# Kernel tuning notes

Measured on AMD Instinct MI355X. Metric: run time of the kernel, lower is better.

## Reference

```python
import jax, jax.numpy as jnp
import numpy as np

E = 800000
D = 64
N = 50000

def setup_inputs() -> dict:
    key = jax.random.key(0)
    k1, k2 = jax.random.split(key)
    src = jax.random.normal(k1, (E, D), dtype=jnp.float32)
    index = jax.random.randint(k2, (E,), 0, N, dtype=jnp.int64)
    return {"src": src, "index": index, "dim": 0, "dim_size": N}

def reference(src, index, dim, dim_size):
    # scatter-mean along dim=0: segment sum divided by per-segment counts
    # (torch_scatter mean clamps count to >= 1 so empty segments stay 0).
    sums = jax.ops.segment_sum(src, index, num_segments=dim_size)  # [N, D]
    counts = jax.ops.segment_sum(jnp.ones((src.shape[0],), dtype=src.dtype),
                                 index, num_segments=dim_size)      # [N]
    denom = jnp.maximum(counts, 1.0)
    return sums / denom[:, None]
```

## Files before the change

kernel.cpp:

```cpp
#include <hip/hip_runtime.h>


typedef unsigned int u32;

__global__ void zero_u32_kernel(u32* __restrict__ p, int n) {
    int i = blockIdx.x * blockDim.x + threadIdx.x;
    int stride = gridDim.x * blockDim.x;
    for (; i < n; i += stride) p[i] = 0u;
}

__global__ void hist_kernel(const int* __restrict__ idx, u32* __restrict__ hist, int E) {
    int i = blockIdx.x * blockDim.x + threadIdx.x;
    int stride = gridDim.x * blockDim.x;
    for (; i < E; i += stride) atomicAdd(&hist[idx[i]], 1u);
}


__global__ void scanA_kernel(const u32* __restrict__ hist, u32* __restrict__ pb, int N) {
    const int b = blockIdx.x, t = threadIdx.x;
    const int base = b * 1024 + t * 4;
    u32 s = 0;
#pragma unroll
    for (int k = 0; k < 4; ++k) { int i = base + k; if (i < N) s += hist[i]; }
#pragma unroll
    for (int d = 32; d > 0; d >>= 1) s += __shfl_down(s, d);
    __shared__ u32 wsum[4];
    int lane = t & 63, wid = t >> 6;
    if (lane == 0) wsum[wid] = s;
    __syncthreads();
    if (t == 0) pb[b] = wsum[0] + wsum[1] + wsum[2] + wsum[3];
}

__global__ void scanB_kernel(u32* __restrict__ pb, u32* __restrict__ ofs, int nblk, int N) {
    if (threadIdx.x == 0 && blockIdx.x == 0) {
        u32 run = 0;
        for (int b = 0; b < nblk; ++b) { u32 v = pb[b]; pb[b] = run; run += v; }
        ofs[N] = run;
    }
}

__global__ void scanC_kernel(const u32* __restrict__ hist, const u32* __restrict__ pb,
                             u32* __restrict__ ofs, int N) {
    const int b = blockIdx.x, t = threadIdx.x;
    const int base = b * 1024 + t * 4;
    u32 v[4]; u32 s = 0;
#pragma unroll
    for (int k = 0; k < 4; ++k) { int i = base + k; v[k] = (i < N) ? hist[i] : 0u; s += v[k]; }
    u32 inc = s;
    int lane = t & 63, wid = t >> 6;
#pragma unroll
    for (int d = 1; d < 64; d <<= 1) { u32 x = __shfl_up(inc, d); if (lane >= d) inc += x; }
    __shared__ u32 wsum[4];
    if (lane == 63) wsum[wid] = inc;
    __syncthreads();
    u32 waveBase = 0;
    for (int w = 0; w < wid; ++w) waveBase += wsum[w];
    u32 run = pb[b] + waveBase + (inc - s);
#pragma unroll
    for (int k = 0; k < 4; ++k) { int i = base + k; if (i < N) ofs[i] = run; run += v[k]; }
}

__global__ void scatter_perm_kernel(const int* __restrict__ idx, const u32* __restrict__ ofs,
                                    u32* __restrict__ ctr, u32* __restrict__ perm, int E) {
    int i = blockIdx.x * blockDim.x + threadIdx.x;
    int stride = gridDim.x * blockDim.x;
    for (; i < E; i += stride) {
        int n = idx[i];
        u32 pos = ofs[n] + atomicAdd(&ctr[n], 1u);
        perm[pos] = (u32)i;
    }
}

__global__ void gather_mean_kernel(const float* __restrict__ src, const u32* __restrict__ perm,
                                   const u32* __restrict__ ofs, float* __restrict__ out, int N) {
    int seg = blockIdx.x * (blockDim.x >> 6) + (threadIdx.x >> 6);
    int lane = threadIdx.x & 63;
    if (seg >= N) return;
    u32 beg = ofs[seg], end = ofs[seg + 1];
    int cnt = (int)(end - beg);
    float acc = 0.f;
    u32 j = beg;
    for (; j + 2 <= end; j += 2) {
        u32 e0 = perm[j], e1 = perm[j + 1];
        acc += src[(long)e0 * 64 + lane];
        acc += src[(long)e1 * 64 + lane];
    }
    if (j < end) acc += src[(long)perm[j] * 64 + lane];
    float inv = 1.0f / (float)(cnt > 1 ? cnt : 1);
    out[(long)seg * 64 + lane] = acc * inv;
}

__global__ void zero_f4_kernel(float4* __restrict__ p, long n4) {
    long i = (long)blockIdx.x * blockDim.x + threadIdx.x;
    long stride = (long)gridDim.x * blockDim.x;
    float4 z = make_float4(0.f, 0.f, 0.f, 0.f);
    for (; i < n4; i += stride) p[i] = z;
}
__global__ void scatter_add_kernel(const float4* __restrict__ src4, const int* __restrict__ idx,
                                   float* __restrict__ out, float* __restrict__ cnt, int E) {
    long t = (long)blockIdx.x * blockDim.x + threadIdx.x;
    long total = (long)E * 16;
    long stride = (long)gridDim.x * blockDim.x;
    for (; t < total; t += stride) {
        int e = (int)(t >> 4), c4 = (int)(t & 15);
        int n = idx[e];
        float4 v = src4[(long)e * 16 + c4];
        float* o = out + (long)n * 64 + c4 * 4;
        atomicAdd(o + 0, v.x); atomicAdd(o + 1, v.y);
        atomicAdd(o + 2, v.z); atomicAdd(o + 3, v.w);
        if (c4 == 0) atomicAdd(cnt + n, 1.0f);
    }
}
__global__ void divide_kernel(float4* __restrict__ out4, const float* __restrict__ cnt, int N) {
    long t = (long)blockIdx.x * blockDim.x + threadIdx.x;
    long total = (long)N * 16;
    long stride = (long)gridDim.x * blockDim.x;
    for (; t < total; t += stride) {
        int n = (int)(t >> 4);
        float inv = 1.0f / fmaxf(cnt[n], 1.0f);
        float4 v = out4[t];
        v.x *= inv; v.y *= inv; v.z *= inv; v.w *= inv;
        out4[t] = v;
    }
}

extern "C" void kernel_launch(void* const* d_in, const int* in_sizes, int n_in,
                              void* d_out, int out_size, void* d_ws, size_t ws_size,
                              hipStream_t stream) {
    const float* src = (const float*)d_in[0];
    const int*   idx = (const int*)d_in[1];
    float* out = (float*)d_out;

    const int E = in_sizes[1];
    const int D = in_sizes[0] / E;
    const int N = out_size / D;
    const int BLK = 256;

    const size_t OFS_OFF  = 0;
    const size_t HIST_OFF = (size_t)(N + 64) & ~63ul;
    const size_t PB_OFF   = HIST_OFF + (((size_t)N + 64) & ~63ul);
    const size_t PERM_OFF = PB_OFF + 64;
    const size_t NEED = (PERM_OFF + (size_t)E) * 4;

    if (ws_size >= NEED) {
        u32* W    = (u32*)d_ws;
        u32* ofs  = W + OFS_OFF;
        u32* hist = W + HIST_OFF;
        u32* pb   = W + PB_OFF;
        u32* perm = W + PERM_OFF;

        const int nblk = (N + 1023) / 1024;

        zero_u32_kernel<<<(N + BLK - 1) / BLK > 2048 ? 2048 : (N + BLK - 1) / BLK, BLK, 0, stream>>>(hist, N);
        {
            int grid = (E + BLK - 1) / BLK; if (grid > 2048) grid = 2048;
            hist_kernel<<<grid, BLK, 0, stream>>>(idx, hist, E);
        }
        scanA_kernel<<<nblk, BLK, 0, stream>>>(hist, pb, N);
        scanB_kernel<<<1, 64, 0, stream>>>(pb, ofs, nblk, N);
        scanC_kernel<<<nblk, BLK, 0, stream>>>(hist, pb, ofs, N);
        {
            int grid = (N + BLK - 1) / BLK; if (grid > 2048) grid = 2048;
            zero_u32_kernel<<<grid, BLK, 0, stream>>>(hist, N);
        }
        {
            int grid = (E + BLK - 1) / BLK; if (grid > 2048) grid = 2048;
            scatter_perm_kernel<<<grid, BLK, 0, stream>>>(idx, ofs, hist, perm, E);
        }
        {
            int segs_per_blk = BLK / 64;
            int grid = (N + segs_per_blk - 1) / segs_per_blk;
            gather_mean_kernel<<<grid, BLK, 0, stream>>>(src, perm, ofs, out, N);
        }
    } else {
        float* cnt = (float*)d_ws;
        {
            long n4 = (long)out_size / 4;
            int grid = (int)((n4 + BLK - 1) / BLK); if (grid > 2048) grid = 2048;
            zero_f4_kernel<<<grid, BLK, 0, stream>>>((float4*)out, n4);
        }
        {
            long n4 = (long)N / 4;
            int grid = (int)((n4 + BLK - 1) / BLK); if (grid > 2048) grid = 2048;
            zero_f4_kernel<<<grid, BLK, 0, stream>>>((float4*)cnt, n4);
        }
        {
            long total = (long)E * 16;
            int grid = (int)((total + BLK - 1) / BLK); if (grid > 2048) grid = 2048;
            scatter_add_kernel<<<grid, BLK, 0, stream>>>((const float4*)src, idx, out, cnt, E);
        }
        {
            long total = (long)N * 16;
            int grid = (int)((total + BLK - 1) / BLK); if (grid > 2048) grid = 2048;
            divide_kernel<<<grid, BLK, 0, stream>>>((float4*)out, cnt, N);
        }
    }
}
```

Before: 417.6 us.

## Record atomic ranks in histogram pass and batch perm loads in gather

After: 355.9 us. 14.8% less time.

```diff
diff --git a/kernel.cpp b/kernel.cpp
--- a/kernel.cpp
+++ b/kernel.cpp
@@ -9,10 +9,13 @@
     for (; i < n; i += stride) p[i] = 0u;
 }
 
-__global__ void hist_kernel(const int* __restrict__ idx, u32* __restrict__ hist, int E) {
+__global__ void hist_rank_kernel(const int* __restrict__ idx, u32* __restrict__ hist,
+                                 u32* __restrict__ rank, int E) {
     int i = blockIdx.x * blockDim.x + threadIdx.x;
     int stride = gridDim.x * blockDim.x;
-    for (; i < E; i += stride) atomicAdd(&hist[idx[i]], 1u);
+    for (; i < E; i += stride) {
+        rank[i] = atomicAdd(&hist[idx[i]], 1u);
+    }
 }
 
 
@@ -60,32 +63,54 @@
     for (int k = 0; k < 4; ++k) { int i = base + k; if (i < N) ofs[i] = run; run += v[k]; }
 }
 
-__global__ void scatter_perm_kernel(const int* __restrict__ idx, const u32* __restrict__ ofs,
-                                    u32* __restrict__ ctr, u32* __restrict__ perm, int E) {
+__global__ void scatter_perm_kernel(const int* __restrict__ idx, const u32* __restrict__ rank,
+                                    const u32* __restrict__ ofs, u32* __restrict__ perm, int E) {
     int i = blockIdx.x * blockDim.x + threadIdx.x;
     int stride = gridDim.x * blockDim.x;
     for (; i < E; i += stride) {
         int n = idx[i];
-        u32 pos = ofs[n] + atomicAdd(&ctr[n], 1u);
-        perm[pos] = (u32)i;
+        perm[ofs[n] + rank[i]] = (u32)i;
     }
 }
 
 __global__ void gather_mean_kernel(const float* __restrict__ src, const u32* __restrict__ perm,
                                    const u32* __restrict__ ofs, float* __restrict__ out, int N) {
     int seg = blockIdx.x * (blockDim.x >> 6) + (threadIdx.x >> 6);
+    if (seg >= N) return;
     int lane = threadIdx.x & 63;
-    if (seg >= N) return;
     u32 beg = ofs[seg], end = ofs[seg + 1];
     int cnt = (int)(end - beg);
     float acc = 0.f;
-    u32 j = beg;
-    for (; j + 2 <= end; j += 2) {
-        u32 e0 = perm[j], e1 = perm[j + 1];
-        acc += src[(long)e0 * 64 + lane];
-        acc += src[(long)e1 * 64 + lane];
-    }
-    if (j < end) acc += src[(long)perm[j] * 64 + lane];
+    int j = 0;
+    while (j < cnt) {
+        int chunk = cnt - j; if (chunk > 64) chunk = 64;
+        u32 myperm = (lane < chunk) ? perm[beg + j + lane] : 0u;
+        int k = 0;
+        for (; k + 8 <= chunk; k += 8) {
+            u32 e0 = __shfl(myperm, k + 0);
+            u32 e1 = __shfl(myperm, k + 1);
+            u32 e2 = __shfl(myperm, k + 2);
+            u32 e3 = __shfl(myperm, k + 3);
+            u32 e4 = __shfl(myperm, k + 4);
+            u32 e5 = __shfl(myperm, k + 5);
+            u32 e6 = __shfl(myperm, k + 6);
+            u32 e7 = __shfl(myperm, k + 7);
+            float v0 = src[(long)e0 * 64 + lane];
+            float v1 = src[(long)e1 * 64 + lane];
+            float v2 = src[(long)e2 * 64 + lane];
+            float v3 = src[(long)e3 * 64 + lane];
+            float v4 = src[(long)e4 * 64 + lane];
+            float v5 = src[(long)e5 * 64 + lane];
+            float v6 = src[(long)e6 * 64 + lane];
+            float v7 = src[(long)e7 * 64 + lane];
+            acc += ((v0 + v1) + (v2 + v3)) + ((v4 + v5) + (v6 + v7));
+        }
+        for (; k < chunk; ++k) {
+            u32 e = __shfl(myperm, k);
+            acc += src[(long)e * 64 + lane];
+        }
+        j += chunk;
+    }
     float inv = 1.0f / (float)(cnt > 1 ? cnt : 1);
     out[(long)seg * 64 + lane] = acc * inv;
 }
@@ -137,9 +162,10 @@
     const int BLK = 256;
 
     const size_t OFS_OFF  = 0;
-    const size_t HIST_OFF = (size_t)(N + 64) & ~63ul;
-    const size_t PB_OFF   = HIST_OFF + (((size_t)N + 64) & ~63ul);
-    const size_t PERM_OFF = PB_OFF + 64;
+    const size_t HIST_OFF = ((size_t)(N + 1) + 63) & ~63ul;
+    const size_t PB_OFF   = HIST_OFF + (((size_t)N + 63) & ~63ul);
+    const size_t RANK_OFF = PB_OFF + 64;
+    const size_t PERM_OFF = RANK_OFF + (size_t)E;
     const size_t NEED = (PERM_OFF + (size_t)E) * 4;
 
     if (ws_size >= NEED) {
@@ -147,25 +173,25 @@
         u32* ofs  = W + OFS_OFF;
         u32* hist = W + HIST_OFF;
         u32* pb   = W + PB_OFF;
+        u32* rank = W + RANK_OFF;
         u32* perm = W + PERM_OFF;
 
         const int nblk = (N + 1023) / 1024;
 
-        zero_u32_kernel<<<(N + BLK - 1) / BLK > 2048 ? 2048 : (N + BLK - 1) / BLK, BLK, 0, stream>>>(hist, N);
-        {
-            int grid = (E + BLK - 1) / BLK; if (grid > 2048) grid = 2048;
-            hist_kernel<<<grid, BLK, 0, stream>>>(idx, hist, E);
+        {
+            int grid = (N + BLK - 1) / BLK;
+            zero_u32_kernel<<<grid, BLK, 0, stream>>>(hist, N);
+        }
+        {
+            int grid = (E + BLK - 1) / BLK;
+            hist_rank_kernel<<<grid, BLK, 0, stream>>>(idx, hist, rank, E);
         }
         scanA_kernel<<<nblk, BLK, 0, stream>>>(hist, pb, N);
         scanB_kernel<<<1, 64, 0, stream>>>(pb, ofs, nblk, N);
         scanC_kernel<<<nblk, BLK, 0, stream>>>(hist, pb, ofs, N);
         {
-            int grid = (N + BLK - 1) / BLK; if (grid > 2048) grid = 2048;
-            zero_u32_kernel<<<grid, BLK, 0, stream>>>(hist, N);
-        }
-        {
-            int grid = (E + BLK - 1) / BLK; if (grid > 2048) grid = 2048;
-            scatter_perm_kernel<<<grid, BLK, 0, stream>>>(idx, ofs, hist, perm, E);
+            int grid = (E + BLK - 1) / BLK;
+            scatter_perm_kernel<<<grid, BLK, 0, stream>>>(idx, rank, ofs, perm, E);
         }
         {
             int segs_per_blk = BLK / 64;
```
